# Performance work log

Measured on AMD Instinct MI355X. Metric: run time of the kernel, lower is better.

The kernel has to match this reference:

```python
import jax, jax.numpy as jnp
import numpy as np

N = 20000      # nodes
E = 640000     # edges
IN = 2         # in_dim
H = 4          # heads
C = 64         # hidden_dim (per-head channels)
ED = 3         # edge_dim
K = 4          # num_clusters
EPS = 1e-16    # PyG softmax eps


def setup_inputs():
    key = jax.random.key(0)
    ks = jax.random.split(key, 32)
    g = lambda i, sh: (jax.random.normal(ks[i], sh, dtype=jnp.float32) * 0.1)
    inp = {
        'x': jax.random.normal(ks[0], (N, IN), dtype=jnp.float32),
        'edge_index': jax.random.randint(ks[1], (2, E), 0, N, dtype=jnp.int64),
        'edge_attr': jax.random.normal(ks[2], (E, ED), dtype=jnp.float32),
        # input_proj
        'Wp': g(3, (IN, C)), 'bp': g(4, (C,)),
        # conv1: in C -> H*C, concat
        'W1': g(5, (C, H * C)), 'We1': g(6, (ED, H * C)),
        'as1': g(7, (H, C)), 'ad1': g(8, (H, C)), 'ae1': g(9, (H, C)), 'b1': g(10, (H * C,)),
        # conv2: in H*C -> H*C, concat
        'W2': g(11, (H * C, H * C)), 'We2': g(12, (ED, H * C)),
        'as2': g(13, (H, C)), 'ad2': g(14, (H, C)), 'ae2': g(15, (H, C)), 'b2': g(16, (H * C,)),
        # conv3: in H*C -> C, heads=1
        'W3': g(17, (H * C, C)), 'We3': g(18, (ED, C)),
        'as3': g(19, (1, C)), 'ad3': g(20, (1, C)), 'ae3': g(21, (1, C)), 'b3': g(22, (C,)),
        # classifier
        'Wc': g(23, (C, K)), 'bc': g(24, (K,)),
    }
    return inp


def _gat(h, src, dst, edge_attr, W, We, a_src, a_dst, a_edge, bias, heads, cph):
    """PyG GATConv (shared lin for src/dst, edge_dim, concat=True), eval mode."""
    xh = (h @ W).reshape(N, heads, cph)                       # [N,H,C]
    alpha_src = jnp.einsum('nhc,hc->nh', xh, a_src)           # [N,H]
    alpha_dst = jnp.einsum('nhc,hc->nh', xh, a_dst)
    eh = (edge_attr @ We).reshape(E, heads, cph)              # [E,H,C]
    alpha = alpha_src[src] + alpha_dst[dst] + jnp.einsum('ehc,hc->eh', eh, a_edge)
    alpha = jax.nn.leaky_relu(alpha, 0.2)                     # [E,H]
    # segment softmax over destination neighborhoods
    m = jax.ops.segment_max(alpha, dst, num_segments=N)       # [N,H]
    ea = jnp.exp(alpha - m[dst])
    s = jax.ops.segment_sum(ea, dst, num_segments=N)
    attn = ea / (s[dst] + EPS)                                # [E,H]
    msg = xh[src] * attn[:, :, None]                          # [E,H,C]
    out = jax.ops.segment_sum(msg, dst, num_segments=N)       # [N,H,C]
    return out.reshape(N, heads * cph) + bias


def reference(x, edge_index, edge_attr, Wp, bp,
              W1, We1, as1, ad1, ae1, b1,
              W2, We2, as2, ad2, ae2, b2,
              W3, We3, as3, ad3, ae3, b3,
              Wc, bc):
    src, dst = edge_index[0], edge_index[1]
    h = jax.nn.elu(x @ Wp + bp)
    h = jax.nn.elu(_gat(h, src, dst, edge_attr, W1, We1, as1, ad1, ae1, b1, H, C))
    h = jax.nn.elu(_gat(h, src, dst, edge_attr, W2, We2, as2, ad2, ae2, b2, H, C))
    h = _gat(h, src, dst, edge_attr, W3, We3, as3, ad3, ae3, b3, 1, C)
    return jax.nn.softmax(h @ Wc + bc, axis=-1)
```

## Files before the change

kernel.cpp:

```cpp
#include <hip/hip_runtime.h>
#include <math.h>

#define N_NODES 20000
#define N_EDGES 640000

typedef __attribute__((ext_vector_type(8))) short short8;
typedef __attribute__((ext_vector_type(4))) float floatx4;

__device__ __forceinline__ float elu_f(float v) { return v > 0.f ? v : expm1f(v); }

__device__ __forceinline__ unsigned short bf16_rne(float f) {
  union { float f; unsigned u; } v;
  v.f = f;
  unsigned r = v.u + 0x7FFF + ((v.u >> 16) & 1);
  return (unsigned short)(r >> 16);
}

__device__ __forceinline__ float bf_to_f(unsigned short u) {
  union { unsigned u; float f; } v;
  v.u = (unsigned)u << 16;
  return v.f;
}

__device__ __forceinline__ int swz(int c) {
  return (c & ~7) | ((((c & 7) + ((c >> 3) >> 2))) & 7);
}


__global__ void zero_int_kernel(int* p, int n) {
  int i = blockIdx.x * 256 + threadIdx.x;
  if (i < n) p[i] = 0;
}

__global__ void hist_kernel(const int* __restrict__ dst, int* __restrict__ cnt, int ne) {
  int e = blockIdx.x * 256 + threadIdx.x;
  if (e < ne) atomicAdd(&cnt[dst[e]], 1);
}

__global__ __launch_bounds__(1024) void scan_kernel(const int* __restrict__ cnt,
                                                    int* __restrict__ row_ptr,
                                                    int* __restrict__ row_next, int n) {
  __shared__ int part[1024];
  int t = threadIdx.x;
  int per = (n + 1023) / 1024;
  int base = t * per;
  int local = 0;
  for (int i = 0; i < per; ++i) {
    int idx = base + i;
    if (idx < n) local += cnt[idx];
  }
  part[t] = local;
  __syncthreads();
  for (int off = 1; off < 1024; off <<= 1) {
    int v = (t >= off) ? part[t - off] : 0;
    __syncthreads();
    part[t] += v;
    __syncthreads();
  }
  int prefix = (t == 0) ? 0 : part[t - 1];
  for (int i = 0; i < per; ++i) {
    int idx = base + i;
    if (idx < n) {
      row_ptr[idx] = prefix;
      row_next[idx] = prefix;
      prefix += cnt[idx];
    }
  }
  if (t == 1023) row_ptr[n] = part[1023];
}

__global__ void fill_kernel(const int* __restrict__ dst, int* __restrict__ row_next,
                            int* __restrict__ csr_eid, int ne) {
  int e = blockIdx.x * 256 + threadIdx.x;
  if (e >= ne) return;
  int pos = atomicAdd(&row_next[dst[e]], 1);
  csr_eid[pos] = e;
}


__global__ void wt_all_kernel(const float* __restrict__ W1, const float* __restrict__ W2,
                              const float* __restrict__ W3, unsigned short* __restrict__ Bt1,
                              unsigned short* __restrict__ Bt2, unsigned short* __restrict__ Bt3) {
  int idx = blockIdx.x * 256 + threadIdx.x;
  const float* W; unsigned short* Bt; int K, Nc, local;
  if (idx < 16384)      { W = W1; Bt = Bt1; K = 64;  Nc = 256; local = idx; }
  else if (idx < 81920) { W = W2; Bt = Bt2; K = 256; Nc = 256; local = idx - 16384; }
  else if (idx < 98304) { W = W3; Bt = Bt3; K = 256; Nc = 64;  local = idx - 81920; }
  else return;
  int k = local / Nc, n = local - k * Nc;
  Bt[(size_t)n * K + k] = bf16_rne(W[local]);
}


__global__ void aeproj_all_kernel(const float* __restrict__ We1, const float* __restrict__ ae1,
                                  const float* __restrict__ We2, const float* __restrict__ ae2,
                                  const float* __restrict__ We3, const float* __restrict__ ae3,
                                  float* __restrict__ proj) {
  int t = threadIdx.x;
  if (t < 12) {
    int d = t >> 2, h = t & 3;
    float s = 0.f;
    for (int c = 0; c < 64; ++c) s += We1[d * 256 + h * 64 + c] * ae1[h * 64 + c];
    proj[t] = s;
  } else if (t < 24) {
    int u = t - 12; int d = u >> 2, h = u & 3;
    float s = 0.f;
    for (int c = 0; c < 64; ++c) s += We2[d * 256 + h * 64 + c] * ae2[h * 64 + c];
    proj[12 + u] = s;
  } else if (t < 27) {
    int d = t - 24;
    float s = 0.f;
    for (int c = 0; c < 64; ++c) s += We3[d * 64 + c] * ae3[c];
    proj[24 + d] = s;
  }
}


__global__ void edge_prep_kernel(const int* __restrict__ csr_eid, const int* __restrict__ src,
                                 const float* __restrict__ ea, const float* __restrict__ proj,
                                 int* __restrict__ csr_src, float* __restrict__ edot) {
  int i = blockIdx.x * 256 + threadIdx.x;
  if (i >= N_EDGES) return;
  int eid = csr_eid[i];
  csr_src[i] = src[eid];
  float e0 = ea[eid * 3 + 0], e1 = ea[eid * 3 + 1], e2 = ea[eid * 3 + 2];
  #pragma unroll
  for (int h = 0; h < 4; ++h)
    edot[(size_t)h * N_EDGES + i] = e0 * proj[h] + e1 * proj[4 + h] + e2 * proj[8 + h];
  #pragma unroll
  for (int h = 0; h < 4; ++h)
    edot[(size_t)(4 + h) * N_EDGES + i] = e0 * proj[12 + h] + e1 * proj[16 + h] + e2 * proj[20 + h];
  edot[(size_t)8 * N_EDGES + i] = e0 * proj[24] + e1 * proj[25] + e2 * proj[26];
}


__global__ void in_proj_kernel(const float* __restrict__ x, const float* __restrict__ Wp,
                               const float* __restrict__ bp, unsigned short* __restrict__ h_bf,
                               int n) {
  int i = blockIdx.x * 256 + threadIdx.x;
  if (i >= n * 64) return;
  int node = i >> 6, c = i & 63;
  float v = x[node * 2] * Wp[c] + x[node * 2 + 1] * Wp[64 + c] + bp[c];
  h_bf[i] = bf16_rne(elu_f(v));
}


template <int KDIM>
__global__ __launch_bounds__(256) void mfma_gemm_alpha_kernel(
    const unsigned short* __restrict__ A, const unsigned short* __restrict__ Bt,
    unsigned short* __restrict__ C_bf, const float* __restrict__ a_src,
    const float* __restrict__ a_dst, float* __restrict__ alp_s,
    float* __restrict__ alp_d, int M, int Nc) {
  __shared__ unsigned short As[64][40];
  __shared__ unsigned short Bs[64][40];
  int t = threadIdx.x;
  int wave = t >> 6, lane = t & 63;
  int m_frag = lane & 15, quad = lane >> 4;
  int row0 = blockIdx.y * 64, col0 = blockIdx.x * 64;
  int lr = t >> 2;
  int lk = (t & 3) * 8;
  floatx4 acc[4];
  #pragma unroll
  for (int c = 0; c < 4; ++c) acc[c] = (floatx4){0.f, 0.f, 0.f, 0.f};

  for (int k0 = 0; k0 < KDIM; k0 += 32) {
    int gr = row0 + lr;
    short8 av = {0, 0, 0, 0, 0, 0, 0, 0};
    if (gr < M) av = *(const short8*)(A + (size_t)gr * KDIM + k0 + lk);
    *(short8*)(&As[lr][lk]) = av;
    short8 bv = *(const short8*)(Bt + (size_t)(col0 + lr) * KDIM + k0 + lk);
    *(short8*)(&Bs[lr][lk]) = bv;
    __syncthreads();
    short8 a = *(const short8*)(&As[wave * 16 + m_frag][quad * 8]);
    #pragma unroll
    for (int c = 0; c < 4; ++c) {
      short8 b = *(const short8*)(&Bs[c * 16 + m_frag][quad * 8]);
      acc[c] = __builtin_amdgcn_mfma_f32_16x16x32_bf16(a, b, acc[c], 0, 0, 0);
    }
    __syncthreads();
  }

  int H = Nc >> 6;
  int head = blockIdx.x;
  float ps[4] = {}, pd[4] = {};
  #pragma unroll
  for (int c = 0; c < 4; ++c) {
    float asv = a_src[head * 64 + c * 16 + m_frag];
    float adv = a_dst[head * 64 + c * 16 + m_frag];
    #pragma unroll
    for (int i = 0; i < 4; ++i) {
      ps[i] += acc[c][i] * asv;
      pd[i] += acc[c][i] * adv;
    }
  }
  #pragma unroll
  for (int off = 1; off < 16; off <<= 1) {
    #pragma unroll
    for (int i = 0; i < 4; ++i) {
      ps[i] += __shfl_xor(ps[i], off);
      pd[i] += __shfl_xor(pd[i], off);
    }
  }
  #pragma unroll
  for (int c = 0; c < 4; ++c) {
    #pragma unroll
    for (int i = 0; i < 4; ++i) {
      int gr = row0 + wave * 16 + quad * 4 + i;
      if (gr < M) C_bf[(size_t)gr * Nc + col0 + c * 16 + m_frag] = bf16_rne(acc[c][i]);
    }
  }
  if (m_frag == 0) {
    #pragma unroll
    for (int i = 0; i < 4; ++i) {
      int gr = row0 + wave * 16 + quad * 4 + i;
      if (gr < M) {
        alp_s[gr * H + head] = ps[i];
        alp_d[gr * H + head] = pd[i];
      }
    }
  }
}


template <int HC, bool APPLY_ELU, bool OUT_BF>
__global__ __launch_bounds__(256) void softagg_kernel(
    const int* __restrict__ row_ptr, const int* __restrict__ csr_src,
    const float* __restrict__ edot, const float* __restrict__ alp_s,
    const float* __restrict__ alp_d, const unsigned short* __restrict__ xh_bf,
    const float* __restrict__ bias, float* __restrict__ out,
    unsigned short* __restrict__ out_bf) {
  constexpr int H = HC / 64;
  constexpr int CHUNK = 256;
  constexpr int L = HC / 8;
  constexpr int S = 256 / L;
  __shared__ float lds_w[H][CHUNK];
  __shared__ int lds_src[CHUNK];
  __shared__ float sh_r[H];
  __shared__ float sh_inv[H];
  __shared__ float red[4 * HC];

  int n = blockIdx.x;
  int t = threadIdx.x;
  int wave = t >> 6, lane = t & 63;
  int slot = t / L, l = t % L;
  int head2 = (8 * l) >> 6;
  int s0 = row_ptr[n], s1 = row_ptr[n + 1];

  float m_run = -INFINITY, s_run = 0.f;
  float acc[8] = {};
  float adv = 0.f;
  const float* __restrict__ edot_h = edot + (size_t)wave * N_EDGES;
  if (wave < H) adv = alp_d[n * H + wave];

  for (int c0 = s0; c0 < s1; c0 += CHUNK) {
    int cend = min(s1, c0 + CHUNK);
    if (wave < H) {
      int h = wave;
      float cm = -INFINITY;
      for (int i = c0 + lane; i < cend; i += 64) {
        int s = csr_src[i];
        if (h == 0) lds_src[i - c0] = s;
        float a = alp_s[s * H + h] + adv + edot_h[i];
        a = a > 0.f ? a : 0.2f * a;
        lds_w[h][i - c0] = a;
        cm = fmaxf(cm, a);
      }
      #pragma unroll
      for (int off = 1; off < 64; off <<= 1) cm = fmaxf(cm, __shfl_xor(cm, off));
      float m_new = fmaxf(m_run, cm);
      float r = __expf(m_run - m_new);
      float se = 0.f;
      for (int i = c0 + lane; i < cend; i += 64) {
        float w = __expf(lds_w[h][i - c0] - m_new);
        lds_w[h][i - c0] = w;
        se += w;
      }
      #pragma unroll
      for (int off = 1; off < 64; off <<= 1) se += __shfl_xor(se, off);
      s_run = s_run * r + se;
      m_run = m_new;
      if (lane == 0) sh_r[h] = r;
    }
    __syncthreads();
    float rr = sh_r[head2];
    #pragma unroll
    for (int j = 0; j < 8; ++j) acc[j] *= rr;
    int i = c0 + slot;
    for (; i + S < cend; i += 2 * S) {
      int sA = lds_src[i - c0];
      int sB = lds_src[i - c0 + S];
      float wA = lds_w[head2][i - c0];
      float wB = lds_w[head2][i - c0 + S];
      short8 vA = *(const short8*)(xh_bf + (size_t)sA * HC + l * 8);
      short8 vB = *(const short8*)(xh_bf + (size_t)sB * HC + l * 8);
      #pragma unroll
      for (int j = 0; j < 8; ++j) acc[j] += bf_to_f((unsigned short)vA[j]) * wA;
      #pragma unroll
      for (int j = 0; j < 8; ++j) acc[j] += bf_to_f((unsigned short)vB[j]) * wB;
    }
    if (i < cend) {
      int s = lds_src[i - c0];
      float w = lds_w[head2][i - c0];
      short8 v = *(const short8*)(xh_bf + (size_t)s * HC + l * 8);
      #pragma unroll
      for (int j = 0; j < 8; ++j) acc[j] += bf_to_f((unsigned short)v[j]) * w;
    }
    __syncthreads();
  }
  if (wave < H && lane == 0) sh_inv[wave] = 1.0f / (s_run + 1e-16f);
  __syncthreads();
  float inv = sh_inv[head2];
  #pragma unroll
  for (int j = 0; j < 8; ++j) acc[j] *= inv;
  #pragma unroll
  for (int off = L; off < 64; off <<= 1) {
    #pragma unroll
    for (int j = 0; j < 8; ++j) acc[j] += __shfl_xor(acc[j], off);
  }
  if (lane < L) {
    #pragma unroll
    for (int j = 0; j < 8; ++j) red[wave * HC + swz(lane * 8 + j)] = acc[j];
  }
  __syncthreads();
  if (t < HC) {
    int pos = swz(t);
    float a = red[0 * HC + pos] + red[1 * HC + pos] + red[2 * HC + pos] + red[3 * HC + pos];
    a += bias[t];
    if (APPLY_ELU) a = elu_f(a);
    if (OUT_BF) out_bf[(size_t)n * HC + t] = bf16_rne(a);
    else out[(size_t)n * HC + t] = a;
  }
}


__global__ void classifier_kernel(const float* __restrict__ h, const float* __restrict__ Wc,
                                  const float* __restrict__ bc, float* __restrict__ out,
                                  int n_nodes) {
  int gid = blockIdx.x * 256 + threadIdx.x;
  int w = gid >> 6, lane = gid & 63;
  if (w >= n_nodes) return;
  float hv = h[w * 64 + lane];
  float p0 = hv * Wc[lane * 4 + 0];
  float p1 = hv * Wc[lane * 4 + 1];
  float p2 = hv * Wc[lane * 4 + 2];
  float p3 = hv * Wc[lane * 4 + 3];
  for (int off = 32; off; off >>= 1) {
    p0 += __shfl_down(p0, off);
    p1 += __shfl_down(p1, off);
    p2 += __shfl_down(p2, off);
    p3 += __shfl_down(p3, off);
  }
  if (lane == 0) {
    p0 += bc[0]; p1 += bc[1]; p2 += bc[2]; p3 += bc[3];
    float mx = fmaxf(fmaxf(p0, p1), fmaxf(p2, p3));
    float e0 = __expf(p0 - mx), e1 = __expf(p1 - mx), e2 = __expf(p2 - mx), e3 = __expf(p3 - mx);
    float inv = 1.f / (e0 + e1 + e2 + e3);
    out[w * 4 + 0] = e0 * inv;
    out[w * 4 + 1] = e1 * inv;
    out[w * 4 + 2] = e2 * inv;
    out[w * 4 + 3] = e3 * inv;
  }
}


extern "C" void kernel_launch(void* const* d_in, const int* in_sizes, int n_in,
                              void* d_out, int out_size, void* d_ws, size_t ws_size,
                              hipStream_t stream) {
  const float* x   = (const float*)d_in[0];
  const int*   ei  = (const int*)d_in[1];
  const float* ea  = (const float*)d_in[2];
  const float* Wp  = (const float*)d_in[3];
  const float* bp  = (const float*)d_in[4];
  const float* W1  = (const float*)d_in[5];
  const float* We1 = (const float*)d_in[6];
  const float* as1 = (const float*)d_in[7];
  const float* ad1 = (const float*)d_in[8];
  const float* ae1 = (const float*)d_in[9];
  const float* b1  = (const float*)d_in[10];
  const float* W2  = (const float*)d_in[11];
  const float* We2 = (const float*)d_in[12];
  const float* as2 = (const float*)d_in[13];
  const float* ad2 = (const float*)d_in[14];
  const float* ae2 = (const float*)d_in[15];
  const float* b2  = (const float*)d_in[16];
  const float* W3  = (const float*)d_in[17];
  const float* We3 = (const float*)d_in[18];
  const float* as3 = (const float*)d_in[19];
  const float* ad3 = (const float*)d_in[20];
  const float* ae3 = (const float*)d_in[21];
  const float* b3  = (const float*)d_in[22];
  const float* Wc  = (const float*)d_in[23];
  const float* bc  = (const float*)d_in[24];
  float* out = (float*)d_out;

  const int* src = ei;
  const int* dst = ei + N_EDGES;

  char* wptr = (char*)d_ws;
  auto alloc = [&](size_t bytes) {
    char* p = wptr;
    wptr += (bytes + 255) & ~(size_t)255;
    return p;
  };
  int*            cnt      = (int*)alloc((size_t)N_NODES * 4);
  int*            row_ptr  = (int*)alloc((size_t)(N_NODES + 1) * 4);
  int*            row_next = (int*)alloc((size_t)N_NODES * 4);
  int*            csr_eid  = (int*)alloc((size_t)N_EDGES * 4);
  int*            csr_src  = (int*)alloc((size_t)N_EDGES * 4);
  float*          edot     = (float*)alloc((size_t)9 * N_EDGES * 4);
  unsigned short* hA_bf    = (unsigned short*)alloc((size_t)N_NODES * 256 * 2);
  unsigned short* hX_bf    = (unsigned short*)alloc((size_t)N_NODES * 256 * 2);
  float*          hC       = (float*)alloc((size_t)N_NODES * 64 * 4);
  float*          alp_s    = (float*)alloc((size_t)N_NODES * 4 * 4);
  float*          alp_d    = (float*)alloc((size_t)N_NODES * 4 * 4);
  float*          proj     = (float*)alloc(32 * 4);
  unsigned short* Bt1      = (unsigned short*)alloc((size_t)64 * 256 * 2);
  unsigned short* Bt2      = (unsigned short*)alloc((size_t)256 * 256 * 2);
  unsigned short* Bt3      = (unsigned short*)alloc((size_t)256 * 64 * 2);

  zero_int_kernel<<<(N_NODES + 255) / 256, 256, 0, stream>>>(cnt, N_NODES);
  hist_kernel<<<(N_EDGES + 255) / 256, 256, 0, stream>>>(dst, cnt, N_EDGES);
  scan_kernel<<<1, 1024, 0, stream>>>(cnt, row_ptr, row_next, N_NODES);
  fill_kernel<<<(N_EDGES + 255) / 256, 256, 0, stream>>>(dst, row_next, csr_eid, N_EDGES);

  wt_all_kernel<<<(98304 + 255) / 256, 256, 0, stream>>>(W1, W2, W3, Bt1, Bt2, Bt3);
  aeproj_all_kernel<<<1, 64, 0, stream>>>(We1, ae1, We2, ae2, We3, ae3, proj);
  edge_prep_kernel<<<(N_EDGES + 255) / 256, 256, 0, stream>>>(csr_eid, src, ea, proj,
                                                              csr_src, edot);

  in_proj_kernel<<<N_NODES * 64 / 256, 256, 0, stream>>>(x, Wp, bp, hA_bf, N_NODES);

  dim3 g256(4, (N_NODES + 63) / 64);
  dim3 g64(1, (N_NODES + 63) / 64);

  mfma_gemm_alpha_kernel<64><<<g256, 256, 0, stream>>>(hA_bf, Bt1, hX_bf, as1, ad1,
                                                       alp_s, alp_d, N_NODES, 256);
  softagg_kernel<256, true, true><<<N_NODES, 256, 0, stream>>>(row_ptr, csr_src,
                                                               edot + (size_t)0 * N_EDGES,
                                                               alp_s, alp_d, hX_bf,
                                                               b1, nullptr, hA_bf);

  mfma_gemm_alpha_kernel<256><<<g256, 256, 0, stream>>>(hA_bf, Bt2, hX_bf, as2, ad2,
                                                        alp_s, alp_d, N_NODES, 256);
  softagg_kernel<256, true, true><<<N_NODES, 256, 0, stream>>>(row_ptr, csr_src,
                                                               edot + (size_t)4 * N_EDGES,
                                                               alp_s, alp_d, hX_bf,
                                                               b2, nullptr, hA_bf);

  mfma_gemm_alpha_kernel<256><<<g64, 256, 0, stream>>>(hA_bf, Bt3, hX_bf, as3, ad3,
                                                       alp_s, alp_d, N_NODES, 64);
  softagg_kernel<64, false, false><<<N_NODES, 256, 0, stream>>>(row_ptr, csr_src,
                                                                edot + (size_t)8 * N_EDGES,
                                                                alp_s, alp_d, hX_bf,
                                                                b3, hC, nullptr);

  classifier_kernel<<<N_NODES * 64 / 256, 256, 0, stream>>>(hC, Wc, bc, out, N_NODES);
}
```

Before: 423.1 us.

## Fuse prep kernels, packed-FMA aggregation, and fuse layer-3 aggregation with classifier

Merges the input projection, weight transpose and edge-projection kernels into one launch. Rewrites the 4-head aggregation to unpack bf16 pairs and accumulate with packed two-wide FMAs, and pads the LDS weight rows. Replaces the single-head layer-3 aggregation, which used a 256-thread block per node with only one active wave, with a wave-per-node kernel that also applies the classifier and softmax. This removes the hC round trip and a launch and makes better use of the hardware in the last layer.

New measurement: 396.3 us. 1.07x faster.

```diff
diff --git a/kernel.cpp b/kernel.cpp
--- a/kernel.cpp
+++ b/kernel.cpp
@@ -6,6 +6,7 @@
 
 typedef __attribute__((ext_vector_type(8))) short short8;
 typedef __attribute__((ext_vector_type(4))) float floatx4;
+typedef __attribute__((ext_vector_type(2))) float float2v;
 
 __device__ __forceinline__ float elu_f(float v) { return v > 0.f ? v : expm1f(v); }
 
@@ -20,6 +21,13 @@
   union { unsigned u; float f; } v;
   v.u = (unsigned)u << 16;
   return v.f;
+}
+
+__device__ __forceinline__ float2v unpack_bf2(unsigned u) {
+  union { unsigned u; float f; } lo, hi;
+  lo.u = u << 16;
+  hi.u = u & 0xffff0000u;
+  return (float2v){lo.f, hi.f};
 }
 
 __device__ __forceinline__ int swz(int c) {
@@ -78,40 +86,47 @@
 }
 
 
-__global__ void wt_all_kernel(const float* __restrict__ W1, const float* __restrict__ W2,
-                              const float* __restrict__ W3, unsigned short* __restrict__ Bt1,
-                              unsigned short* __restrict__ Bt2, unsigned short* __restrict__ Bt3) {
-  int idx = blockIdx.x * 256 + threadIdx.x;
-  const float* W; unsigned short* Bt; int K, Nc, local;
-  if (idx < 16384)      { W = W1; Bt = Bt1; K = 64;  Nc = 256; local = idx; }
-  else if (idx < 81920) { W = W2; Bt = Bt2; K = 256; Nc = 256; local = idx - 16384; }
-  else if (idx < 98304) { W = W3; Bt = Bt3; K = 256; Nc = 64;  local = idx - 81920; }
-  else return;
-  int k = local / Nc, n = local - k * Nc;
-  Bt[(size_t)n * K + k] = bf16_rne(W[local]);
-}
-
-
-__global__ void aeproj_all_kernel(const float* __restrict__ We1, const float* __restrict__ ae1,
-                                  const float* __restrict__ We2, const float* __restrict__ ae2,
-                                  const float* __restrict__ We3, const float* __restrict__ ae3,
-                                  float* __restrict__ proj) {
-  int t = threadIdx.x;
-  if (t < 12) {
-    int d = t >> 2, h = t & 3;
-    float s = 0.f;
-    for (int c = 0; c < 64; ++c) s += We1[d * 256 + h * 64 + c] * ae1[h * 64 + c];
-    proj[t] = s;
-  } else if (t < 24) {
-    int u = t - 12; int d = u >> 2, h = u & 3;
-    float s = 0.f;
-    for (int c = 0; c < 64; ++c) s += We2[d * 256 + h * 64 + c] * ae2[h * 64 + c];
-    proj[12 + u] = s;
-  } else if (t < 27) {
-    int d = t - 24;
-    float s = 0.f;
-    for (int c = 0; c < 64; ++c) s += We3[d * 64 + c] * ae3[c];
-    proj[24 + d] = s;
+__global__ void prep_all_kernel(const float* __restrict__ x, const float* __restrict__ Wp,
+                                const float* __restrict__ bp, unsigned short* __restrict__ h_bf,
+                                const float* __restrict__ W1, const float* __restrict__ W2,
+                                const float* __restrict__ W3, unsigned short* __restrict__ Bt1,
+                                unsigned short* __restrict__ Bt2, unsigned short* __restrict__ Bt3,
+                                const float* __restrict__ We1, const float* __restrict__ ae1,
+                                const float* __restrict__ We2, const float* __restrict__ ae2,
+                                const float* __restrict__ We3, const float* __restrict__ ae3,
+                                float* __restrict__ proj) {
+  int b = blockIdx.x, t = threadIdx.x;
+  if (b < 5000) {
+    int i = b * 256 + t;
+    int node = i >> 6, c = i & 63;
+    float v = x[node * 2] * Wp[c] + x[node * 2 + 1] * Wp[64 + c] + bp[c];
+    h_bf[i] = bf16_rne(elu_f(v));
+  } else if (b < 5384) {
+    int idx = (b - 5000) * 256 + t;
+    const float* W; unsigned short* Bt; int K, Nc, local;
+    if (idx < 16384)      { W = W1; Bt = Bt1; K = 64;  Nc = 256; local = idx; }
+    else if (idx < 81920) { W = W2; Bt = Bt2; K = 256; Nc = 256; local = idx - 16384; }
+    else if (idx < 98304) { W = W3; Bt = Bt3; K = 256; Nc = 64;  local = idx - 81920; }
+    else return;
+    int k = local / Nc, n = local - k * Nc;
+    Bt[(size_t)n * K + k] = bf16_rne(W[local]);
+  } else {
+    if (t < 12) {
+      int d = t >> 2, h = t & 3;
+      float s = 0.f;
+      for (int c = 0; c < 64; ++c) s += We1[d * 256 + h * 64 + c] * ae1[h * 64 + c];
+      proj[t] = s;
+    } else if (t < 24) {
+      int u = t - 12; int d = u >> 2, h = u & 3;
+      float s = 0.f;
+      for (int c = 0; c < 64; ++c) s += We2[d * 256 + h * 64 + c] * ae2[h * 64 + c];
+      proj[12 + u] = s;
+    } else if (t < 27) {
+      int d = t - 24;
+      float s = 0.f;
+      for (int c = 0; c < 64; ++c) s += We3[d * 64 + c] * ae3[c];
+      proj[24 + d] = s;
+    }
   }
 }
 
@@ -131,17 +146,6 @@
   for (int h = 0; h < 4; ++h)
     edot[(size_t)(4 + h) * N_EDGES + i] = e0 * proj[12 + h] + e1 * proj[16 + h] + e2 * proj[20 + h];
   edot[(size_t)8 * N_EDGES + i] = e0 * proj[24] + e1 * proj[25] + e2 * proj[26];
-}
-
-
-__global__ void in_proj_kernel(const float* __restrict__ x, const float* __restrict__ Wp,
-                               const float* __restrict__ bp, unsigned short* __restrict__ h_bf,
-                               int n) {
-  int i = blockIdx.x * 256 + threadIdx.x;
-  if (i >= n * 64) return;
-  int node = i >> 6, c = i & 63;
-  float v = x[node * 2] * Wp[c] + x[node * 2 + 1] * Wp[64 + c] + bp[c];
-  h_bf[i] = bf16_rne(elu_f(v));
 }
 
 
@@ -222,18 +226,15 @@
 }
 
 
-template <int HC, bool APPLY_ELU, bool OUT_BF>
-__global__ __launch_bounds__(256) void softagg_kernel(
+template <bool OUT_BF>
+__global__ __launch_bounds__(256) void softagg4_kernel(
     const int* __restrict__ row_ptr, const int* __restrict__ csr_src,
     const float* __restrict__ edot, const float* __restrict__ alp_s,
     const float* __restrict__ alp_d, const unsigned short* __restrict__ xh_bf,
     const float* __restrict__ bias, float* __restrict__ out,
     unsigned short* __restrict__ out_bf) {
-  constexpr int H = HC / 64;
-  constexpr int CHUNK = 256;
-  constexpr int L = HC / 8;
-  constexpr int S = 256 / L;
-  __shared__ float lds_w[H][CHUNK];
+  constexpr int HC = 256, H = 4, CHUNK = 256, L = 32, S = 8;
+  __shared__ float lds_w[H][CHUNK + 8];
   __shared__ int lds_src[CHUNK];
   __shared__ float sh_r[H];
   __shared__ float sh_inv[H];
@@ -247,14 +248,13 @@
   int s0 = row_ptr[n], s1 = row_ptr[n + 1];
 
   float m_run = -INFINITY, s_run = 0.f;
-  float acc[8] = {};
-  float adv = 0.f;
+  float2v accp[4] = {};
+  float adv = alp_d[n * H + wave];
   const float* __restrict__ edot_h = edot + (size_t)wave * N_EDGES;
-  if (wave < H) adv = alp_d[n * H + wave];
 
   for (int c0 = s0; c0 < s1; c0 += CHUNK) {
     int cend = min(s1, c0 + CHUNK);
-    if (wave < H) {
+    {
       int h = wave;
       float cm = -INFINITY;
       for (int i = c0 + lane; i < cend; i += 64) {
@@ -282,83 +282,165 @@
       if (lane == 0) sh_r[h] = r;
     }
     __syncthreads();
-    float rr = sh_r[head2];
-    #pragma unroll
-    for (int j = 0; j < 8; ++j) acc[j] *= rr;
+    float2v rrp = {sh_r[head2], sh_r[head2]};
+    #pragma unroll
+    for (int d = 0; d < 4; ++d) accp[d] *= rrp;
     int i = c0 + slot;
     for (; i + S < cend; i += 2 * S) {
       int sA = lds_src[i - c0];
       int sB = lds_src[i - c0 + S];
       float wA = lds_w[head2][i - c0];
       float wB = lds_w[head2][i - c0 + S];
-      short8 vA = *(const short8*)(xh_bf + (size_t)sA * HC + l * 8);
-      short8 vB = *(const short8*)(xh_bf + (size_t)sB * HC + l * 8);
-      #pragma unroll
-      for (int j = 0; j < 8; ++j) acc[j] += bf_to_f((unsigned short)vA[j]) * wA;
-      #pragma unroll
-      for (int j = 0; j < 8; ++j) acc[j] += bf_to_f((unsigned short)vB[j]) * wB;
+      uint4 uA = *(const uint4*)(xh_bf + (size_t)sA * HC + l * 8);
+      uint4 uB = *(const uint4*)(xh_bf + (size_t)sB * HC + l * 8);
+      float2v wAp = {wA, wA}, wBp = {wB, wB};
+      accp[0] = __builtin_elementwise_fma(unpack_bf2(uA.x), wAp, accp[0]);
+      accp[1] = __builtin_elementwise_fma(unpack_bf2(uA.y), wAp, accp[1]);
+      accp[2] = __builtin_elementwise_fma(unpack_bf2(uA.z), wAp, accp[2]);
+      accp[3] = __builtin_elementwise_fma(unpack_bf2(uA.w), wAp, accp[3]);
+      accp[0] = __builtin_elementwise_fma(unpack_bf2(uB.x), wBp, accp[0]);
+      accp[1] = __builtin_elementwise_fma(unpack_bf2(uB.y), wBp, accp[1]);
+      accp[2] = __builtin_elementwise_fma(unpack_bf2(uB.z), wBp, accp[2]);
+      accp[3] = __builtin_elementwise_fma(unpack_bf2(uB.w), wBp, accp[3]);
     }
     if (i < cend) {
       int s = lds_src[i - c0];
       float w = lds_w[head2][i - c0];
-      short8 v = *(const short8*)(xh_bf + (size_t)s * HC + l * 8);
-      #pragma unroll
-      for (int j = 0; j < 8; ++j) acc[j] += bf_to_f((unsigned short)v[j]) * w;
+      uint4 u = *(const uint4*)(xh_bf + (size_t)s * HC + l * 8);
+      float2v wp = {w, w};
+      accp[0] = __builtin_elementwise_fma(unpack_bf2(u.x), wp, accp[0]);
+      accp[1] = __builtin_elementwise_fma(unpack_bf2(u.y), wp, accp[1]);
+      accp[2] = __builtin_elementwise_fma(unpack_bf2(u.z), wp, accp[2]);
+      accp[3] = __builtin_elementwise_fma(unpack_bf2(u.w), wp, accp[3]);
     }
     __syncthreads();
   }
-  if (wave < H && lane == 0) sh_inv[wave] = 1.0f / (s_run + 1e-16f);
+  if (lane == 0) sh_inv[wave] = 1.0f / (s_run + 1e-16f);
   __syncthreads();
-  float inv = sh_inv[head2];
-  #pragma unroll
-  for (int j = 0; j < 8; ++j) acc[j] *= inv;
+  float2v invp = {sh_inv[head2], sh_inv[head2]};
+  #pragma unroll
+  for (int d = 0; d < 4; ++d) accp[d] *= invp;
+  float accf[8];
+  #pragma unroll
+  for (int d = 0; d < 4; ++d) { accf[2 * d] = accp[d].x; accf[2 * d + 1] = accp[d].y; }
   #pragma unroll
   for (int off = L; off < 64; off <<= 1) {
     #pragma unroll
-    for (int j = 0; j < 8; ++j) acc[j] += __shfl_xor(acc[j], off);
+    for (int j = 0; j < 8; ++j) accf[j] += __shfl_xor(accf[j], off);
   }
   if (lane < L) {
     #pragma unroll
-    for (int j = 0; j < 8; ++j) red[wave * HC + swz(lane * 8 + j)] = acc[j];
+    for (int j = 0; j < 8; ++j) red[wave * HC + swz(lane * 8 + j)] = accf[j];
   }
   __syncthreads();
-  if (t < HC) {
-    int pos = swz(t);
+  {
+    int pos = swz(t & (HC - 1));
     float a = red[0 * HC + pos] + red[1 * HC + pos] + red[2 * HC + pos] + red[3 * HC + pos];
     a += bias[t];
-    if (APPLY_ELU) a = elu_f(a);
+    a = elu_f(a);
     if (OUT_BF) out_bf[(size_t)n * HC + t] = bf16_rne(a);
     else out[(size_t)n * HC + t] = a;
   }
 }
 
 
-__global__ void classifier_kernel(const float* __restrict__ h, const float* __restrict__ Wc,
-                                  const float* __restrict__ bc, float* __restrict__ out,
-                                  int n_nodes) {
-  int gid = blockIdx.x * 256 + threadIdx.x;
-  int w = gid >> 6, lane = gid & 63;
-  if (w >= n_nodes) return;
-  float hv = h[w * 64 + lane];
-  float p0 = hv * Wc[lane * 4 + 0];
-  float p1 = hv * Wc[lane * 4 + 1];
-  float p2 = hv * Wc[lane * 4 + 2];
-  float p3 = hv * Wc[lane * 4 + 3];
-  for (int off = 32; off; off >>= 1) {
-    p0 += __shfl_down(p0, off);
-    p1 += __shfl_down(p1, off);
-    p2 += __shfl_down(p2, off);
-    p3 += __shfl_down(p3, off);
+__global__ __launch_bounds__(256) void softagg_cls_kernel(
+    const int* __restrict__ row_ptr, const int* __restrict__ csr_src,
+    const float* __restrict__ edot, const float* __restrict__ alp_s,
+    const float* __restrict__ alp_d, const unsigned short* __restrict__ xh_bf,
+    const float* __restrict__ b3, const float* __restrict__ Wc,
+    const float* __restrict__ bc, float* __restrict__ out, int n_nodes) {
+  constexpr int CHUNK = 256;
+  __shared__ float lds_w[4][CHUNK];
+  __shared__ int lds_s[4][CHUNK];
+
+  int wave = threadIdx.x >> 6, lane = threadIdx.x & 63;
+  int n = blockIdx.x * 4 + wave;
+  if (n >= n_nodes) return;
+  int slot = lane >> 3, l = lane & 7;
+  int s0 = row_ptr[n], s1 = row_ptr[n + 1];
+
+  float m_run = -INFINITY, s_run = 0.f;
+  float2v accp[4] = {};
+  float adv = alp_d[n];
+
+  for (int c0 = s0; c0 < s1; c0 += CHUNK) {
+    int cend = min(s1, c0 + CHUNK);
+    float cm = -INFINITY;
+    for (int i = c0 + lane; i < cend; i += 64) {
+      int s = csr_src[i];
+      lds_s[wave][i - c0] = s;
+      float a = alp_s[s] + adv + edot[i];
+      a = a > 0.f ? a : 0.2f * a;
+      lds_w[wave][i - c0] = a;
+      cm = fmaxf(cm, a);
+    }
+    #pragma unroll
+    for (int off = 1; off < 64; off <<= 1) cm = fmaxf(cm, __shfl_xor(cm, off));
+    float m_new = fmaxf(m_run, cm);
+    float r = __expf(m_run - m_new);
+    float se = 0.f;
+    for (int i = c0 + lane; i < cend; i += 64) {
+      float w = __expf(lds_w[wave][i - c0] - m_new);
+      lds_w[wave][i - c0] = w;
+      se += w;
+    }
+    #pragma unroll
+    for (int off = 1; off < 64; off <<= 1) se += __shfl_xor(se, off);
+    s_run = s_run * r + se;
+    m_run = m_new;
+    float2v rp = {r, r};
+    #pragma unroll
+    for (int d = 0; d < 4; ++d) accp[d] *= rp;
+    for (int i = c0 + slot; i < cend; i += 8) {
+      int s = lds_s[wave][i - c0];
+      float w = lds_w[wave][i - c0];
+      uint4 u = *(const uint4*)(xh_bf + (size_t)s * 64 + l * 8);
+      float2v wp = {w, w};
+      accp[0] = __builtin_elementwise_fma(unpack_bf2(u.x), wp, accp[0]);
+      accp[1] = __builtin_elementwise_fma(unpack_bf2(u.y), wp, accp[1]);
+      accp[2] = __builtin_elementwise_fma(unpack_bf2(u.z), wp, accp[2]);
+      accp[3] = __builtin_elementwise_fma(unpack_bf2(u.w), wp, accp[3]);
+    }
+  }
+  float inv = 1.0f / (s_run + 1e-16f);
+  float2v invp = {inv, inv};
+  #pragma unroll
+  for (int d = 0; d < 4; ++d) accp[d] *= invp;
+  float accf[8];
+  #pragma unroll
+  for (int d = 0; d < 4; ++d) { accf[2 * d] = accp[d].x; accf[2 * d + 1] = accp[d].y; }
+  #pragma unroll
+  for (int off = 8; off < 64; off <<= 1) {
+    #pragma unroll
+    for (int j = 0; j < 8; ++j) accf[j] += __shfl_xor(accf[j], off);
+  }
+  float p0 = 0.f, p1 = 0.f, p2 = 0.f, p3 = 0.f;
+  #pragma unroll
+  for (int j = 0; j < 8; ++j) {
+    int c = l * 8 + j;
+    float v = accf[j] + b3[c];
+    p0 += v * Wc[c * 4 + 0];
+    p1 += v * Wc[c * 4 + 1];
+    p2 += v * Wc[c * 4 + 2];
+    p3 += v * Wc[c * 4 + 3];
+  }
+  #pragma unroll
+  for (int off = 1; off < 8; off <<= 1) {
+    p0 += __shfl_xor(p0, off);
+    p1 += __shfl_xor(p1, off);
+    p2 += __shfl_xor(p2, off);
+    p3 += __shfl_xor(p3, off);
   }
   if (lane == 0) {
     p0 += bc[0]; p1 += bc[1]; p2 += bc[2]; p3 += bc[3];
     float mx = fmaxf(fmaxf(p0, p1), fmaxf(p2, p3));
     float e0 = __expf(p0 - mx), e1 = __expf(p1 - mx), e2 = __expf(p2 - mx), e3 = __expf(p3 - mx);
-    float inv = 1.f / (e0 + e1 + e2 + e3);
-    out[w * 4 + 0] = e0 * inv;
-    out[w * 4 + 1] = e1 * inv;
-    out[w * 4 + 2] = e2 * inv;
-    out[w * 4 + 3] = e3 * inv;
+    float s = 1.f / (e0 + e1 + e2 + e3);
+    out[n * 4 + 0] = e0 * s;
+    out[n * 4 + 1] = e1 * s;
+    out[n * 4 + 2] = e2 * s;
+    out[n * 4 + 3] = e3 * s;
   }
 }
 
@@ -410,7 +492,6 @@
   float*          edot     = (float*)alloc((size_t)9 * N_EDGES * 4);
   unsigned short* hA_bf    = (unsigned short*)alloc((size_t)N_NODES * 256 * 2);
   unsigned short* hX_bf    = (unsigned short*)alloc((size_t)N_NODES * 256 * 2);
-  float*          hC       = (float*)alloc((size_t)N_NODES * 64 * 4);
   float*          alp_s    = (float*)alloc((size_t)N_NODES * 4 * 4);
   float*          alp_d    = (float*)alloc((size_t)N_NODES * 4 * 4);
   float*          proj     = (float*)alloc(32 * 4);
@@ -423,36 +504,30 @@
   scan_kernel<<<1, 1024, 0, stream>>>(cnt, row_ptr, row_next, N_NODES);
   fill_kernel<<<(N_EDGES + 255) / 256, 256, 0, stream>>>(dst, row_next, csr_eid, N_EDGES);
 
-  wt_all_kernel<<<(98304 + 255) / 256, 256, 0, stream>>>(W1, W2, W3, Bt1, Bt2, Bt3);
-  aeproj_all_kernel<<<1, 64, 0, stream>>>(We1, ae1, We2, ae2, We3, ae3, proj);
+  prep_all_kernel<<<5385, 256, 0, stream>>>(x, Wp, bp, hA_bf, W1, W2, W3, Bt1, Bt2, Bt3,
+                                            We1, ae1, We2, ae2, We3, ae3, proj);
   edge_prep_kernel<<<(N_EDGES + 255) / 256, 256, 0, stream>>>(csr_eid, src, ea, proj,
                                                               csr_src, edot);
 
-  in_proj_kernel<<<N_NODES * 64 / 256, 256, 0, stream>>>(x, Wp, bp, hA_bf, N_NODES);
-
   dim3 g256(4, (N_NODES + 63) / 64);
   dim3 g64(1, (N_NODES + 63) / 64);
 
   mfma_gemm_alpha_kernel<64><<<g256, 256, 0, stream>>>(hA_bf, Bt1, hX_bf, as1, ad1,
                                                        alp_s, alp_d, N_NODES, 256);
-  softagg_kernel<256, true, true><<<N_NODES, 256, 0, stream>>>(row_ptr, csr_src,
-                                                               edot + (size_t)0 * N_EDGES,
-                                                               alp_s, alp_d, hX_bf,
-                                                               b1, nullptr, hA_bf);
+  softagg4_kernel<true><<<N_NODES, 256, 0, stream>>>(row_ptr, csr_src,
+                                                     edot + (size_t)0 * N_EDGES,
+                                                     alp_s, alp_d, hX_bf, b1, nullptr, hA_bf);
 
   mfma_gemm_alpha_kernel<256><<<g256, 256, 0, stream>>>(hA_bf, Bt2, hX_bf, as2, ad2,
                                                         alp_s, alp_d, N_NODES, 256);
-  softagg_kernel<256, true, true><<<N_NODES, 256, 0, stream>>>(row_ptr, csr_src,
-                                                               edot + (size_t)4 * N_EDGES,
-                                                               alp_s, alp_d, hX_bf,
-                                                               b2, nullptr, hA_bf);
+  softagg4_kernel<true><<<N_NODES, 256, 0, stream>>>(row_ptr, csr_src,
+                                                     edot + (size_t)4 * N_EDGES,
+                                                     alp_s, alp_d, hX_bf, b2, nullptr, hA_bf);
 
   mfma_gemm_alpha_kernel<256><<<g64, 256, 0, stream>>>(hA_bf, Bt3, hX_bf, as3, ad3,
                                                        alp_s, alp_d, N_NODES, 64);
-  softagg_kernel<64, false, false><<<N_NODES, 256, 0, stream>>>(row_ptr, csr_src,
-                                                                edot + (size_t)8 * N_EDGES,
-                                                                alp_s, alp_d, hX_bf,
-                                                                b3, hC, nullptr);
-
-  classifier_kernel<<<N_NODES * 64 / 256, 256, 0, stream>>>(hC, Wc, bc, out, N_NODES);
-}
+  softagg_cls_kernel<<<(N_NODES + 3) / 4, 256, 0, stream>>>(row_ptr, csr_src,
+                                                            edot + (size_t)8 * N_EDGES,
+                                                            alp_s, alp_d, hX_bf, b3, Wc, bc,
+                                                            out, N_NODES);
+}
```
